# Kernel optimization log

Hardware: AMD Instinct MI355X
Metric: run time of the kernel (lower is better)

Reference implementation:

```python
import jax, jax.numpy as jnp
import numpy as np

H = 64            # hidden_size
HORIZON = 168     # forecast_horizon = 7*24


def lstm_cell(x, h, c, Wih, Whh, bih, bhh):
    # PyTorch LSTM gate order: i, f, g, o
    g = x @ Wih.T + bih + h @ Whh.T + bhh          # [B, 4H]
    i, f, gg, o = jnp.split(g, 4, axis=-1)
    i = jax.nn.sigmoid(i)
    f = jax.nn.sigmoid(f)
    gg = jnp.tanh(gg)
    o = jax.nn.sigmoid(o)
    c_new = f * c + i * gg
    h_new = o * jnp.tanh(c_new)
    return h_new, c_new


def run_layer(xs, Wih, Whh, bih, bhh):
    # xs: [T, B, in] -> (hs [T, B, H], h_final, c_final), zero initial state
    B = xs.shape[1]
    h0 = jnp.zeros((B, H), xs.dtype)
    c0 = jnp.zeros((B, H), xs.dtype)

    def step(carry, x_t):
        h, c = carry
        h, c = lstm_cell(x_t, h, c, Wih, Whh, bih, bhh)
        return (h, c), h

    (hf, cf), hs = jax.lax.scan(step, (h0, c0), xs)
    return hs, hf, cf


def setup_inputs() -> dict:
    key = jax.random.key(0)
    ks = iter(jax.random.split(key, 32))
    B, T, IN = 8192, 336, 1
    bound = 1.0 / np.sqrt(H)  # PyTorch default LSTM init scale

    def u(shape):
        return jax.random.uniform(next(ks), shape, jnp.float32, -bound, bound)

    def lstm_params(in_dim):
        return u((4 * H, in_dim)), u((4 * H, H)), u((4 * H,)), u((4 * H,))

    enc_Wih0, enc_Whh0, enc_bih0, enc_bhh0 = lstm_params(IN)
    enc_Wih1, enc_Whh1, enc_bih1, enc_bhh1 = lstm_params(H)
    dec_Wih0, dec_Whh0, dec_bih0, dec_bhh0 = lstm_params(H)
    dec_Wih1, dec_Whh1, dec_bih1, dec_bhh1 = lstm_params(H)
    fc_W = u((1, H))
    fc_b = u((1,))

    x = jax.random.normal(next(ks), (B, T, IN), jnp.float32)
    return dict(
        x=x,
        enc_Wih0=enc_Wih0, enc_Whh0=enc_Whh0, enc_bih0=enc_bih0, enc_bhh0=enc_bhh0,
        enc_Wih1=enc_Wih1, enc_Whh1=enc_Whh1, enc_bih1=enc_bih1, enc_bhh1=enc_bhh1,
        dec_Wih0=dec_Wih0, dec_Whh0=dec_Whh0, dec_bih0=dec_bih0, dec_bhh0=dec_bhh0,
        dec_Wih1=dec_Wih1, dec_Whh1=dec_Whh1, dec_bih1=dec_bih1, dec_bhh1=dec_bhh1,
        fc_W=fc_W, fc_b=fc_b,
    )


def reference(x,
              enc_Wih0, enc_Whh0, enc_bih0, enc_bhh0,
              enc_Wih1, enc_Whh1, enc_bih1, enc_bhh1,
              dec_Wih0, dec_Whh0, dec_bih0, dec_bhh0,
              dec_Wih1, dec_Whh1, dec_bih1, dec_bhh1,
              fc_W, fc_b):
    B = x.shape[0]
    xs = jnp.swapaxes(x, 0, 1)                      # [T, B, 1]

    # Encoder: 2-layer LSTM, keep final (h, c) per layer
    hs0, h0f, c0f = run_layer(xs, enc_Wih0, enc_Whh0, enc_bih0, enc_bhh0)
    _, h1f, c1f = run_layer(hs0, enc_Wih1, enc_Whh1, enc_bih1, enc_bhh1)

    dec_in0 = jnp.zeros((B, H), x.dtype)

    def dstep(carry, _):
        h0, c0, h1, c1, xin = carry
        h0, c0 = lstm_cell(xin, h0, c0, dec_Wih0, dec_Whh0, dec_bih0, dec_bhh0)
        h1, c1 = lstm_cell(h0, h1, c1, dec_Wih1, dec_Whh1, dec_bih1, dec_bhh1)
        pred = h1 @ fc_W.T + fc_b                   # [B, 1]
        return (h0, c0, h1, c1, h1), pred

    _, preds = jax.lax.scan(dstep, (h0f, c0f, h1f, c1f, dec_in0), None, length=HORIZON)
    return jnp.swapaxes(preds, 0, 1)                # [B, 168, 1]
```

## Files before the change

### kernel.cpp

```cpp
#include <hip/hip_runtime.h>


#define TT  336
#define HZN 168
#define NT  512
#define ROWS 16
#define XP  340
#define LN2E 1.44269504088896340736f
#define K2  2.88539008177792681472f

typedef short s8v __attribute__((ext_vector_type(8)));
typedef float f4v __attribute__((ext_vector_type(4)));
typedef float f2v __attribute__((ext_vector_type(2)));

#define MF(wf, hf, c) __builtin_amdgcn_mfma_f32_16x16x32_bf16((wf), (hf), (c), 0, 0, 0)

__device__ __forceinline__ short bf16rne(float f){
  unsigned u = __float_as_uint(f);
  return (short)((u + 0x7fffu + ((u >> 16) & 1u)) >> 16);
}

__device__ __forceinline__ f2v prcp(f2v d){
  return f2v{__builtin_amdgcn_rcpf(d.x), __builtin_amdgcn_rcpf(d.y)};
}
__device__ __forceinline__ f2v pexp2(f2v d){
  return f2v{__builtin_amdgcn_exp2f(d.x), __builtin_amdgcn_exp2f(d.y)};
}

__device__ __forceinline__ s8v ldW(const float* __restrict__ Wm, int w, int l,
                                   int mt, int kt){
  int mm   = l & 15;
  int grow = (mm & 3)*64 + w*8 + 2*(mm >> 2) + mt;
  int k0   = kt*32 + (l >> 4)*8;
  const float* p = Wm + grow*64 + k0;
  float4 q0 = *(const float4*)(p);
  float4 q1 = *(const float4*)(p + 4);
  s8v v;
  v[0]=bf16rne(q0.x*LN2E); v[1]=bf16rne(q0.y*LN2E);
  v[2]=bf16rne(q0.z*LN2E); v[3]=bf16rne(q0.w*LN2E);
  v[4]=bf16rne(q1.x*LN2E); v[5]=bf16rne(q1.y*LN2E);
  v[6]=bf16rne(q1.z*LN2E); v[7]=bf16rne(q1.w*LN2E);
  return v;
}

__device__ __forceinline__ void pwise2(f4v aA, f4v aB, f2v& c2,
                                       float& hA, float& hB){
  f2v i2{aA[0], aB[0]}, f2{aA[1], aB[1]}, g2{aA[2], aB[2]}, o2{aA[3], aB[3]};
  f2v ei = pexp2(-i2);
  f2v ef = pexp2(-f2);
  f2v eg = pexp2(g2 + g2);
  f2v eo = pexp2(-o2);
  f2v ig = (eg - 1.f) * prcp((1.f + ei) * (1.f + eg));
  f2v cn = c2 * prcp(1.f + ef) + ig;
  f2v ec = pexp2(cn * K2);
  f2v h  = (ec - 1.f) * prcp((1.f + eo) * (1.f + ec));
  c2 = cn;
  hA = h.x; hB = h.y;
}

__device__ __forceinline__ void stH2(short* dst, float hA, float hB){
  unsigned pk;
  asm("v_cvt_pk_bf16_f32 %0, %1, %2" : "=v"(pk) : "v"(hA), "v"(hB));
  *(unsigned*)dst = pk;
}

#define ENC_SUPER(P, t, DO_L0) {                                            \
  const short* h0R  = hS + (P)*2048;                                        \
  short*       h0Wr = hS + ((P)^1)*2048;                                    \
  const short* h1R  = hS + 4096 + (P)*2048;                                 \
  short*       h1Wr = hS + 4096 + ((P)^1)*2048;                             \
  s8v g00 = *(const s8v*)(h0R + lo0), g01 = *(const s8v*)(h0R + lo1);       \
  {                                                                         \
    s8v g10 = *(const s8v*)(h1R + lo0), g11 = *(const s8v*)(h1R + lo1);     \
    f4v aA = bE1a, aB = bE1b;                                               \
    aA = MF(Wih1[0][0], g00, aA); aB = MF(Wih1[1][0], g00, aB);             \
    aA = MF(Wih1[0][1], g01, aA); aB = MF(Wih1[1][1], g01, aB);             \
    aA = MF(Whh1[0][0], g10, aA); aB = MF(Whh1[1][0], g10, aB);             \
    aA = MF(Whh1[0][1], g11, aA); aB = MF(Whh1[1][1], g11, aB);             \
    float h1a, h1b;                                                         \
    pwise2(aA, aB, c1s, h1a, h1b);                                          \
    stH2(h1Wr + so, h1a, h1b);                                              \
  }                                                                         \
  if (DO_L0){                                                               \
    float xv = xs[b*XP + (t) + 1];                                          \
    f4v aC = bE0a + wxa*xv;                                                 \
    f4v aD = bE0b + wxb*xv;                                                 \
    aC = MF(Whh0[0][0], g00, aC); aD = MF(Whh0[1][0], g00, aD);             \
    aC = MF(Whh0[0][1], g01, aC); aD = MF(Whh0[1][1], g01, aD);             \
    float h0a, h0b;                                                         \
    pwise2(aC, aD, c0s, h0a, h0b);                                          \
    stH2(h0Wr + so, h0a, h0b);                                              \
  }                                                                         \
  __syncthreads();                                                          \
}

#define DEC_STEP(Q, s) {                                                    \
  const short* h0R  = hS + (Q)*2048;                                        \
  short*       h0Wr = hS + ((Q)^1)*2048;                                    \
  const short* h1R  = hS + 4096 + ((Q)^1)*2048;                             \
  short*       h1Wr = hS + 4096 + (Q)*2048;                                 \
  s8v e0 = *(const s8v*)(h1R + lo0), e1 = *(const s8v*)(h1R + lo1);         \
  {                                                                         \
    f4v aA = *(const f4v*)(bD0L + c0*4);                                    \
    f4v aB = *(const f4v*)(bD0L + c0*4 + 4);                                \
    s8v f0 = *(const s8v*)(h0R + lo0), f1 = *(const s8v*)(h0R + lo1);       \
    aA = MF(Whh0[0][0], f0, aA); aB = MF(Whh0[1][0], f0, aB);               \
    aA = MF(Whh0[0][1], f1, aA); aB = MF(Whh0[1][1], f1, aB);               \
    if ((s) > 0){                                                           \
      aA = MF(Dih0[0][0], e0, aA); aB = MF(Dih0[1][0], e0, aB);             \
      aA = MF(Dih0[0][1], e1, aA); aB = MF(Dih0[1][1], e1, aB);             \
    }                                                                       \
    float h0a, h0b;                                                         \
    pwise2(aA, aB, c0s, h0a, h0b);                                          \
    stH2(h0Wr + so, h0a, h0b);                                              \
  }                                                                         \
  __syncthreads();                                                          \
  {                                                                         \
    f4v aA = *(const f4v*)(bD1L + c0*4);                                    \
    f4v aB = *(const f4v*)(bD1L + c0*4 + 4);                                \
    s8v g0 = *(const s8v*)(h0Wr + lo0), g1 = *(const s8v*)(h0Wr + lo1);     \
    aA = MF(Wih1[0][0], g0, aA); aB = MF(Wih1[1][0], g0, aB);               \
    aA = MF(Wih1[0][1], g1, aA); aB = MF(Wih1[1][1], g1, aB);               \
    aA = MF(Whh1[0][0], e0, aA); aB = MF(Whh1[1][0], e0, aB);               \
    aA = MF(Whh1[0][1], e1, aA); aB = MF(Whh1[1][1], e1, aB);               \
    float h1a, h1b;                                                         \
    pwise2(aA, aB, c1s, h1a, h1b);                                          \
    stH2(h1Wr + so, h1a, h1b);                                              \
    float pr = h1a*fcwA + h1b*fcwB;                                         \
    pr += __shfl_xor(pr, 16); pr += __shfl_xor(pr, 32);                     \
    if (l < 16) fcred[l*9 + w] = pr;                                        \
  }                                                                         \
  __syncthreads();                                                          \
  if (tid < 16){                                                            \
    float sm2 = fcb0;                                                       \
    _Pragma("unroll")                                                       \
    for (int j=0; j<8; j++) sm2 += fcred[tid*9 + j];                        \
    out[(size_t)(brow0 + tid)*HZN + (s)] = sm2;                             \
  }                                                                         \
}

__global__ __launch_bounds__(NT, 4)
void edlstm_kernel(const float* __restrict__ x,
  const float* __restrict__ eWih0, const float* __restrict__ eWhh0,
  const float* __restrict__ ebih0, const float* __restrict__ ebhh0,
  const float* __restrict__ eWih1, const float* __restrict__ eWhh1,
  const float* __restrict__ ebih1, const float* __restrict__ ebhh1,
  const float* __restrict__ dWih0, const float* __restrict__ dWhh0,
  const float* __restrict__ dbih0, const float* __restrict__ dbhh0,
  const float* __restrict__ dWih1, const float* __restrict__ dWhh1,
  const float* __restrict__ dbih1, const float* __restrict__ dbhh1,
  const float* __restrict__ fcW, const float* __restrict__ fcb,
  float* __restrict__ out)
{
  __shared__ float xs[ROWS*XP];
  __shared__ short hS[8192];
  __shared__ float fcred[16*9];
  __shared__ float bD0L[256], bD1L[256];

  const int tid = threadIdx.x;
  const int l   = tid & 63;
  const int w   = tid >> 6;
  const int b   = l & 15;
  const int c0  = w*8 + 2*(l >> 4);
  const int brow0 = blockIdx.x * ROWS;

  const int lo0 = b*64 + ((((l >> 4)    ) ^ (b & 7)) << 3);
  const int lo1 = b*64 + (((4 + (l >> 4)) ^ (b & 7)) << 3);
  const int so  = b*64 + (((c0 >> 3) ^ (b & 7)) << 3) + (c0 & 7);

  {
    int4* hz = (int4*)hS;
    #pragma unroll
    for (int k=0; k<2; k++) hz[k*NT + tid] = int4{0,0,0,0};
  }
  #pragma unroll
  for (int k=0; k<3; k++){
    int idx = k*NT + tid;
    if (idx < ROWS*84){
      int row = idx / 84;
      int c   = idx - row*84;
      *(float4*)(xs + row*XP + c*4) =
        *(const float4*)(x + (size_t)(brow0+row)*TT + c*4);
    }
  }
  if (tid < 256){
    int c = tid >> 2, g = tid & 3;
    int j = g*64 + c;
    bD0L[tid] = (dbih0[j] + dbhh0[j]) * LN2E;
    bD1L[tid] = (dbih1[j] + dbhh1[j]) * LN2E;
  }

  f4v bE0a, bE0b, bE1a, bE1b, wxa, wxb;
  #pragma unroll
  for (int g2=0; g2<4; g2++){
    int j = g2*64 + c0;
    bE0a[g2] = (ebih0[j]   + ebhh0[j])   * LN2E;
    bE0b[g2] = (ebih0[j+1] + ebhh0[j+1]) * LN2E;
    bE1a[g2] = (ebih1[j]   + ebhh1[j])   * LN2E;
    bE1b[g2] = (ebih1[j+1] + ebhh1[j+1]) * LN2E;
    wxa[g2]  = eWih0[j]   * LN2E;
    wxb[g2]  = eWih0[j+1] * LN2E;
  }

  s8v Whh0[2][2], Wih1[2][2], Whh1[2][2];
  #pragma unroll
  for (int mt=0; mt<2; mt++)
    #pragma unroll
    for (int kt=0; kt<2; kt++){
      Whh0[mt][kt] = ldW(eWhh0, w, l, mt, kt);
      Wih1[mt][kt] = ldW(eWih1, w, l, mt, kt);
      Whh1[mt][kt] = ldW(eWhh1, w, l, mt, kt);
    }

  f2v c0s = {0.f, 0.f}, c1s = {0.f, 0.f};
  __syncthreads();

  {
    float xv = xs[b*XP];
    f4v aA = bE0a + wxa*xv;
    f4v aB = bE0b + wxb*xv;
    float h0a, h0b;
    pwise2(aA, aB, c0s, h0a, h0b);
    stH2(hS + 2048 + so, h0a, h0b);
    __syncthreads();
  }

  for (int k=0; k<167; k++){
    ENC_SUPER(1, 2*k,   1);
    ENC_SUPER(0, 2*k+1, 1);
  }
  ENC_SUPER(1, 334, 1);
  ENC_SUPER(0, 335, 0);

  s8v Dih0[2][2];
  #pragma unroll
  for (int mt=0; mt<2; mt++)
    #pragma unroll
    for (int kt=0; kt<2; kt++){
      Dih0[mt][kt] = ldW(dWih0, w, l, mt, kt);
      Whh0[mt][kt] = ldW(dWhh0, w, l, mt, kt);
      Wih1[mt][kt] = ldW(dWih1, w, l, mt, kt);
      Whh1[mt][kt] = ldW(dWhh1, w, l, mt, kt);
    }
  const float fcwA = fcW[c0], fcwB = fcW[c0+1], fcb0 = fcb[0];

  for (int k=0; k<84; k++){
    DEC_STEP(0, 2*k);
    DEC_STEP(1, 2*k+1);
  }
}

extern "C" void kernel_launch(void* const* d_in, const int* in_sizes, int n_in,
                              void* d_out, int out_size, void* d_ws, size_t ws_size,
                              hipStream_t stream)
{
  (void)in_sizes; (void)n_in; (void)d_ws; (void)ws_size; (void)out_size;
  const float* x     = (const float*)d_in[0];
  const float* eWih0 = (const float*)d_in[1];
  const float* eWhh0 = (const float*)d_in[2];
  const float* ebih0 = (const float*)d_in[3];
  const float* ebhh0 = (const float*)d_in[4];
  const float* eWih1 = (const float*)d_in[5];
  const float* eWhh1 = (const float*)d_in[6];
  const float* ebih1 = (const float*)d_in[7];
  const float* ebhh1 = (const float*)d_in[8];
  const float* dWih0 = (const float*)d_in[9];
  const float* dWhh0 = (const float*)d_in[10];
  const float* dbih0 = (const float*)d_in[11];
  const float* dbhh0 = (const float*)d_in[12];
  const float* dWih1 = (const float*)d_in[13];
  const float* dWhh1 = (const float*)d_in[14];
  const float* dbih1 = (const float*)d_in[15];
  const float* dbhh1 = (const float*)d_in[16];
  const float* fcW   = (const float*)d_in[17];
  const float* fcb   = (const float*)d_in[18];
  float* out = (float*)d_out;

  edlstm_kernel<<<dim3(512), dim3(NT), 0, stream>>>(
      x, eWih0, eWhh0, ebih0, ebhh0, eWih1, eWhh1, ebih1, ebhh1,
      dWih0, dWhh0, dbih0, dbhh0, dWih1, dWhh1, dbih1, dbhh1,
      fcW, fcb, out);
}
```

Before: 639.7 us.

## Halve block to 4 waves, each wave computing 16 hidden units per step

```diff
diff --git a/kernel.cpp b/kernel.cpp
--- a/kernel.cpp
+++ b/kernel.cpp
@@ -3,7 +3,7 @@
 
 #define TT  336
 #define HZN 168
-#define NT  512
+#define NT  256
 #define ROWS 16
 #define XP  340
 #define LN2E 1.44269504088896340736f
@@ -19,7 +19,6 @@
   unsigned u = __float_as_uint(f);
   return (short)((u + 0x7fffu + ((u >> 16) & 1u)) >> 16);
 }
-
 __device__ __forceinline__ f2v prcp(f2v d){
   return f2v{__builtin_amdgcn_rcpf(d.x), __builtin_amdgcn_rcpf(d.y)};
 }
@@ -30,7 +29,7 @@
 __device__ __forceinline__ s8v ldW(const float* __restrict__ Wm, int w, int l,
                                    int mt, int kt){
   int mm   = l & 15;
-  int grow = (mm & 3)*64 + w*8 + 2*(mm >> 2) + mt;
+  int grow = (mm & 3)*64 + w*16 + 4*(mm >> 2) + mt;
   int k0   = kt*32 + (l >> 4)*8;
   const float* p = Wm + grow*64 + k0;
   float4 q0 = *(const float4*)(p);
@@ -58,10 +57,12 @@
   hA = h.x; hB = h.y;
 }
 
-__device__ __forceinline__ void stH2(short* dst, float hA, float hB){
-  unsigned pk;
-  asm("v_cvt_pk_bf16_f32 %0, %1, %2" : "=v"(pk) : "v"(hA), "v"(hB));
-  *(unsigned*)dst = pk;
+__device__ __forceinline__ void stH4(short* dst, float h0, float h1,
+                                     float h2, float h3){
+  unsigned pk0, pk1;
+  asm("v_cvt_pk_bf16_f32 %0, %1, %2" : "=v"(pk0) : "v"(h0), "v"(h1));
+  asm("v_cvt_pk_bf16_f32 %0, %1, %2" : "=v"(pk1) : "v"(h2), "v"(h3));
+  *(uint2*)dst = uint2{pk0, pk1};
 }
 
 #define ENC_SUPER(P, t, DO_L0) {                                            \
@@ -72,24 +73,33 @@
   s8v g00 = *(const s8v*)(h0R + lo0), g01 = *(const s8v*)(h0R + lo1);       \
   {                                                                         \
     s8v g10 = *(const s8v*)(h1R + lo0), g11 = *(const s8v*)(h1R + lo1);     \
-    f4v aA = bE1a, aB = bE1b;                                               \
-    aA = MF(Wih1[0][0], g00, aA); aB = MF(Wih1[1][0], g00, aB);             \
-    aA = MF(Wih1[0][1], g01, aA); aB = MF(Wih1[1][1], g01, aB);             \
-    aA = MF(Whh1[0][0], g10, aA); aB = MF(Whh1[1][0], g10, aB);             \
-    aA = MF(Whh1[0][1], g11, aA); aB = MF(Whh1[1][1], g11, aB);             \
-    float h1a, h1b;                                                         \
-    pwise2(aA, aB, c1s, h1a, h1b);                                          \
-    stH2(h1Wr + so, h1a, h1b);                                              \
+    f4v aL[4];                                                              \
+    _Pragma("unroll")                                                       \
+    for (int mt=0; mt<4; mt++){                                             \
+      aL[mt] = bE1[mt];                                                     \
+      aL[mt] = MF(Wih1[mt][0], g00, aL[mt]);                                \
+      aL[mt] = MF(Wih1[mt][1], g01, aL[mt]);                                \
+      aL[mt] = MF(Whh1[mt][0], g10, aL[mt]);                                \
+      aL[mt] = MF(Whh1[mt][1], g11, aL[mt]);                                \
+    }                                                                       \
+    float ha, hb, hc, hd;                                                   \
+    pwise2(aL[0], aL[1], c1s01, ha, hb);                                    \
+    pwise2(aL[2], aL[3], c1s23, hc, hd);                                    \
+    stH4(h1Wr + so, ha, hb, hc, hd);                                        \
   }                                                                         \
   if (DO_L0){                                                               \
     float xv = xs[b*XP + (t) + 1];                                          \
-    f4v aC = bE0a + wxa*xv;                                                 \
-    f4v aD = bE0b + wxb*xv;                                                 \
-    aC = MF(Whh0[0][0], g00, aC); aD = MF(Whh0[1][0], g00, aD);             \
-    aC = MF(Whh0[0][1], g01, aC); aD = MF(Whh0[1][1], g01, aD);             \
-    float h0a, h0b;                                                         \
-    pwise2(aC, aD, c0s, h0a, h0b);                                          \
-    stH2(h0Wr + so, h0a, h0b);                                              \
+    f4v aL[4];                                                              \
+    _Pragma("unroll")                                                       \
+    for (int mt=0; mt<4; mt++){                                             \
+      aL[mt] = bE0[mt] + wx[mt]*xv;                                         \
+      aL[mt] = MF(Whh0[mt][0], g00, aL[mt]);                                \
+      aL[mt] = MF(Whh0[mt][1], g01, aL[mt]);                                \
+    }                                                                       \
+    float ha, hb, hc, hd;                                                   \
+    pwise2(aL[0], aL[1], c0s01, ha, hb);                                    \
+    pwise2(aL[2], aL[3], c0s23, hc, hd);                                    \
+    stH4(h0Wr + so, ha, hb, hc, hd);                                        \
   }                                                                         \
   __syncthreads();                                                          \
 }
@@ -101,45 +111,56 @@
   short*       h1Wr = hS + 4096 + (Q)*2048;                                 \
   s8v e0 = *(const s8v*)(h1R + lo0), e1 = *(const s8v*)(h1R + lo1);         \
   {                                                                         \
-    f4v aA = *(const f4v*)(bD0L + c0*4);                                    \
-    f4v aB = *(const f4v*)(bD0L + c0*4 + 4);                                \
     s8v f0 = *(const s8v*)(h0R + lo0), f1 = *(const s8v*)(h0R + lo1);       \
-    aA = MF(Whh0[0][0], f0, aA); aB = MF(Whh0[1][0], f0, aB);               \
-    aA = MF(Whh0[0][1], f1, aA); aB = MF(Whh0[1][1], f1, aB);               \
+    f4v aL[4];                                                              \
+    _Pragma("unroll")                                                       \
+    for (int mt=0; mt<4; mt++){                                             \
+      aL[mt] = bD0[mt];                                                     \
+      aL[mt] = MF(Whh0[mt][0], f0, aL[mt]);                                 \
+      aL[mt] = MF(Whh0[mt][1], f1, aL[mt]);                                 \
+    }                                                                       \
     if ((s) > 0){                                                           \
-      aA = MF(Dih0[0][0], e0, aA); aB = MF(Dih0[1][0], e0, aB);             \
-      aA = MF(Dih0[0][1], e1, aA); aB = MF(Dih0[1][1], e1, aB);             \
-    }                                                                       \
-    float h0a, h0b;                                                         \
-    pwise2(aA, aB, c0s, h0a, h0b);                                          \
-    stH2(h0Wr + so, h0a, h0b);                                              \
+      _Pragma("unroll")                                                     \
+      for (int mt=0; mt<4; mt++){                                           \
+        aL[mt] = MF(Dih0[mt][0], e0, aL[mt]);                               \
+        aL[mt] = MF(Dih0[mt][1], e1, aL[mt]);                               \
+      }                                                                     \
+    }                                                                       \
+    float ha, hb, hc, hd;                                                   \
+    pwise2(aL[0], aL[1], c0s01, ha, hb);                                    \
+    pwise2(aL[2], aL[3], c0s23, hc, hd);                                    \
+    stH4(h0Wr + so, ha, hb, hc, hd);                                        \
   }                                                                         \
   __syncthreads();                                                          \
   {                                                                         \
-    f4v aA = *(const f4v*)(bD1L + c0*4);                                    \
-    f4v aB = *(const f4v*)(bD1L + c0*4 + 4);                                \
     s8v g0 = *(const s8v*)(h0Wr + lo0), g1 = *(const s8v*)(h0Wr + lo1);     \
-    aA = MF(Wih1[0][0], g0, aA); aB = MF(Wih1[1][0], g0, aB);               \
-    aA = MF(Wih1[0][1], g1, aA); aB = MF(Wih1[1][1], g1, aB);               \
-    aA = MF(Whh1[0][0], e0, aA); aB = MF(Whh1[1][0], e0, aB);               \
-    aA = MF(Whh1[0][1], e1, aA); aB = MF(Whh1[1][1], e1, aB);               \
-    float h1a, h1b;                                                         \
-    pwise2(aA, aB, c1s, h1a, h1b);                                          \
-    stH2(h1Wr + so, h1a, h1b);                                              \
-    float pr = h1a*fcwA + h1b*fcwB;                                         \
+    f4v aL[4];                                                              \
+    _Pragma("unroll")                                                       \
+    for (int mt=0; mt<4; mt++){                                             \
+      aL[mt] = bD1[mt];                                                     \
+      aL[mt] = MF(Wih1[mt][0], g0, aL[mt]);                                 \
+      aL[mt] = MF(Wih1[mt][1], g1, aL[mt]);                                 \
+      aL[mt] = MF(Whh1[mt][0], e0, aL[mt]);                                 \
+      aL[mt] = MF(Whh1[mt][1], e1, aL[mt]);                                 \
+    }                                                                       \
+    float ha, hb, hc, hd;                                                   \
+    pwise2(aL[0], aL[1], c1s01, ha, hb);                                    \
+    pwise2(aL[2], aL[3], c1s23, hc, hd);                                    \
+    stH4(h1Wr + so, ha, hb, hc, hd);                                        \
+    float pr = ha*fcw[0] + hb*fcw[1] + hc*fcw[2] + hd*fcw[3];               \
     pr += __shfl_xor(pr, 16); pr += __shfl_xor(pr, 32);                     \
-    if (l < 16) fcred[l*9 + w] = pr;                                        \
+    if (l < 16) fcred[l*5 + w] = pr;                                        \
   }                                                                         \
   __syncthreads();                                                          \
   if (tid < 16){                                                            \
     float sm2 = fcb0;                                                       \
     _Pragma("unroll")                                                       \
-    for (int j=0; j<8; j++) sm2 += fcred[tid*9 + j];                        \
+    for (int j=0; j<4; j++) sm2 += fcred[tid*5 + j];                        \
     out[(size_t)(brow0 + tid)*HZN + (s)] = sm2;                             \
   }                                                                         \
 }
 
-__global__ __launch_bounds__(NT, 4)
+__global__ __launch_bounds__(NT, 2)
 void edlstm_kernel(const float* __restrict__ x,
   const float* __restrict__ eWih0, const float* __restrict__ eWhh0,
   const float* __restrict__ ebih0, const float* __restrict__ ebhh0,
@@ -154,27 +175,27 @@
 {
   __shared__ float xs[ROWS*XP];
   __shared__ short hS[8192];
-  __shared__ float fcred[16*9];
-  __shared__ float bD0L[256], bD1L[256];
+  __shared__ float fcred[16*5];
 
   const int tid = threadIdx.x;
   const int l   = tid & 63;
   const int w   = tid >> 6;
   const int b   = l & 15;
-  const int c0  = w*8 + 2*(l >> 4);
+  const int lq  = l >> 4;
+  const int c0  = w*16 + 4*lq;
   const int brow0 = blockIdx.x * ROWS;
 
-  const int lo0 = b*64 + ((((l >> 4)    ) ^ (b & 7)) << 3);
-  const int lo1 = b*64 + (((4 + (l >> 4)) ^ (b & 7)) << 3);
+  const int lo0 = b*64 + ((lq       ^ (b & 7)) << 3);
+  const int lo1 = b*64 + (((4 + lq) ^ (b & 7)) << 3);
   const int so  = b*64 + (((c0 >> 3) ^ (b & 7)) << 3) + (c0 & 7);
 
   {
     int4* hz = (int4*)hS;
     #pragma unroll
-    for (int k=0; k<2; k++) hz[k*NT + tid] = int4{0,0,0,0};
-  }
-  #pragma unroll
-  for (int k=0; k<3; k++){
+    for (int k=0; k<4; k++) hz[k*NT + tid] = int4{0,0,0,0};
+  }
+  #pragma unroll
+  for (int k=0; k<6; k++){
     int idx = k*NT + tid;
     if (idx < ROWS*84){
       int row = idx / 84;
@@ -183,28 +204,21 @@
         *(const float4*)(x + (size_t)(brow0+row)*TT + c*4);
     }
   }
-  if (tid < 256){
-    int c = tid >> 2, g = tid & 3;
-    int j = g*64 + c;
-    bD0L[tid] = (dbih0[j] + dbhh0[j]) * LN2E;
-    bD1L[tid] = (dbih1[j] + dbhh1[j]) * LN2E;
-  }
-
-  f4v bE0a, bE0b, bE1a, bE1b, wxa, wxb;
-  #pragma unroll
-  for (int g2=0; g2<4; g2++){
-    int j = g2*64 + c0;
-    bE0a[g2] = (ebih0[j]   + ebhh0[j])   * LN2E;
-    bE0b[g2] = (ebih0[j+1] + ebhh0[j+1]) * LN2E;
-    bE1a[g2] = (ebih1[j]   + ebhh1[j])   * LN2E;
-    bE1b[g2] = (ebih1[j+1] + ebhh1[j+1]) * LN2E;
-    wxa[g2]  = eWih0[j]   * LN2E;
-    wxb[g2]  = eWih0[j+1] * LN2E;
-  }
-
-  s8v Whh0[2][2], Wih1[2][2], Whh1[2][2];
-  #pragma unroll
-  for (int mt=0; mt<2; mt++)
+
+  f4v bE0[4], bE1[4], wx[4];
+  #pragma unroll
+  for (int mt=0; mt<4; mt++)
+    #pragma unroll
+    for (int g2=0; g2<4; g2++){
+      int j = g2*64 + c0 + mt;
+      bE0[mt][g2] = (ebih0[j] + ebhh0[j]) * LN2E;
+      bE1[mt][g2] = (ebih1[j] + ebhh1[j]) * LN2E;
+      wx[mt][g2]  = eWih0[j] * LN2E;
+    }
+
+  s8v Whh0[4][2], Wih1[4][2], Whh1[4][2];
+  #pragma unroll
+  for (int mt=0; mt<4; mt++)
     #pragma unroll
     for (int kt=0; kt<2; kt++){
       Whh0[mt][kt] = ldW(eWhh0, w, l, mt, kt);
@@ -212,16 +226,19 @@
       Whh1[mt][kt] = ldW(eWhh1, w, l, mt, kt);
     }
 
-  f2v c0s = {0.f, 0.f}, c1s = {0.f, 0.f};
+  f2v c0s01 = {0.f,0.f}, c0s23 = {0.f,0.f};
+  f2v c1s01 = {0.f,0.f}, c1s23 = {0.f,0.f};
   __syncthreads();
 
   {
     float xv = xs[b*XP];
-    f4v aA = bE0a + wxa*xv;
-    f4v aB = bE0b + wxb*xv;
-    float h0a, h0b;
-    pwise2(aA, aB, c0s, h0a, h0b);
-    stH2(hS + 2048 + so, h0a, h0b);
+    f4v aL[4];
+    float ha, hb, hc, hd;
+    #pragma unroll
+    for (int mt=0; mt<4; mt++) aL[mt] = bE0[mt] + wx[mt]*xv;
+    pwise2(aL[0], aL[1], c0s01, ha, hb);
+    pwise2(aL[2], aL[3], c0s23, hc, hd);
+    stH4(hS + 2048 + so, ha, hb, hc, hd);
     __syncthreads();
   }
 
@@ -232,9 +249,9 @@
   ENC_SUPER(1, 334, 1);
   ENC_SUPER(0, 335, 0);
 
-  s8v Dih0[2][2];
-  #pragma unroll
-  for (int mt=0; mt<2; mt++)
+  s8v Dih0[4][2];
+  #pragma unroll
+  for (int mt=0; mt<4; mt++)
     #pragma unroll
     for (int kt=0; kt<2; kt++){
       Dih0[mt][kt] = ldW(dWih0, w, l, mt, kt);
@@ -242,7 +259,19 @@
       Wih1[mt][kt] = ldW(dWih1, w, l, mt, kt);
       Whh1[mt][kt] = ldW(dWhh1, w, l, mt, kt);
     }
-  const float fcwA = fcW[c0], fcwB = fcW[c0+1], fcb0 = fcb[0];
+  f4v bD0[4], bD1[4];
+  #pragma unroll
+  for (int mt=0; mt<4; mt++)
+    #pragma unroll
+    for (int g2=0; g2<4; g2++){
+      int j = g2*64 + c0 + mt;
+      bD0[mt][g2] = (dbih0[j] + dbhh0[j]) * LN2E;
+      bD1[mt][g2] = (dbih1[j] + dbhh1[j]) * LN2E;
+    }
+  f4v fcw;
+  #pragma unroll
+  for (int mt=0; mt<4; mt++) fcw[mt] = fcW[c0 + mt];
+  const float fcb0 = fcb[0];
 
   for (int k=0; k<84; k++){
     DEC_STEP(0, 2*k);
```

Result: no change. 652.0 us (+1.9%).
